# Optimization experiments

Hardware: AMD Instinct MI355X
Metric: run time of the kernel (lower is better)

## Reference

```python
import jax, jax.numpy as jnp
import numpy as np

B, N, C = 8, 1025, 768
NUM_HEADS = 12
HEAD_DIM = C // NUM_HEADS  # 64, also depthwise-conv channel count
HW = (32, 32)              # N = 1 + 32*32 (cls token)
SCALE = HEAD_DIM ** -0.5
VALUE_MASK_FILL = -10000.0
LN_EPS = 1e-5


def setup_inputs() -> dict:
    key = jax.random.key(0)
    ks = jax.random.split(key, 12)
    s = 0.02
    inp = {
        "x": jax.random.normal(ks[0], (B, N, C), jnp.float32),
        "mask": jax.random.bernoulli(ks[1], 0.9, (B, N)),
        "Wq": jax.random.normal(ks[2], (C, C), jnp.float32) * s,
        "Wk": jax.random.normal(ks[3], (C, C), jnp.float32) * s,
        "Wv": jax.random.normal(ks[4], (C, C), jnp.float32) * s,
        "pool_q_w": jax.random.normal(ks[5], (HEAD_DIM, 1, 3, 3), jnp.float32) * s,
        "pool_k_w": jax.random.normal(ks[6], (HEAD_DIM, 1, 3, 3), jnp.float32) * s,
        "pool_v_w": jax.random.normal(ks[7], (HEAD_DIM, 1, 3, 3), jnp.float32) * s,
        "gq": jnp.ones((HEAD_DIM,), jnp.float32),
        "bq": jnp.zeros((HEAD_DIM,), jnp.float32),
        "gk": jnp.ones((HEAD_DIM,), jnp.float32),
        "bk": jnp.zeros((HEAD_DIM,), jnp.float32),
        "gv": jnp.ones((HEAD_DIM,), jnp.float32),
        "bv": jnp.zeros((HEAD_DIM,), jnp.float32),
        "Wp": jax.random.normal(ks[8], (C, C), jnp.float32) * s,
        "bp": jnp.zeros((C,), jnp.float32),
    }
    return inp


def _layernorm(t, g, b):
    m = jnp.mean(t, axis=-1, keepdims=True)
    v = jnp.var(t, axis=-1, keepdims=True)
    return (t - m) * jax.lax.rsqrt(v + LN_EPS) * g + b


def _depthwise(t, w):
    # t: [BH, D, H, W], w: [D, 1, 3, 3] depthwise, stride 1, SAME padding
    return jax.lax.conv_general_dilated(
        t, w, window_strides=(1, 1), padding="SAME",
        dimension_numbers=("NCHW", "OIHW", "NCHW"),
        feature_group_count=t.shape[1])


def _attn_pool(t, w, g, b):
    # t: [B, H, N, D] with leading cls token; pool spatial tokens, norm after
    Bb, Hh, Nn, D = t.shape
    cls_tok, spat = t[:, :, :1], t[:, :, 1:]
    Hs, Ws = HW
    spat = spat.reshape(Bb * Hh, Hs, Ws, D).transpose(0, 3, 1, 2)
    spat = _depthwise(spat, w)
    spat = spat.reshape(Bb, Hh, D, Hs * Ws).transpose(0, 1, 3, 2)
    t = jnp.concatenate([cls_tok, spat], axis=2)
    return _layernorm(t, g, b)


def reference(x, mask, Wq, Wk, Wv, pool_q_w, pool_k_w, pool_v_w,
              gq, bq, gk, bk, gv, bv, Wp, bp):
    Bb, Nn, Cc = x.shape
    # QKV projections (no bias), split heads -> [B, H, N, D]
    q = (x @ Wq.T).reshape(Bb, Nn, NUM_HEADS, HEAD_DIM).transpose(0, 2, 1, 3)
    k = (x @ Wk.T).reshape(Bb, Nn, NUM_HEADS, HEAD_DIM).transpose(0, 2, 1, 3)
    v = (x @ Wv.T).reshape(Bb, Nn, NUM_HEADS, HEAD_DIM).transpose(0, 2, 1, 3)
    q = _attn_pool(q, pool_q_w, gq, bq)
    k = _attn_pool(k, pool_k_w, gk, bk)
    v = _attn_pool(v, pool_v_w, gv, bv)
    attn = jnp.einsum("bhqd,bhkd->bhqk", q, k) * SCALE
    # mask: [B, N] bool; broadcast as (B,1,N,1), False -> value_mask_fill
    attn = jnp.where(mask[:, None, :, None], attn, VALUE_MASK_FILL)
    attn = jax.nn.softmax(attn, axis=-1)
    attn_origin = attn
    out = jnp.einsum("bhqk,bhkd->bhqd", attn, v)
    # residual pooling, skipping the cls token
    out = jnp.concatenate([out[:, :, :1], out[:, :, 1:] + q[:, :, 1:]], axis=2)
    out = out.transpose(0, 2, 1, 3).reshape(Bb, Nn, Cc)
    out = out @ Wp.T + bp
    return out, attn_origin
```

## Files before the change

kernel.cpp:

```cpp
#include <hip/hip_runtime.h>
#include <hip/hip_bf16.h>
#include <cstdint>
#include <cstddef>

typedef unsigned short u16;
typedef __attribute__((ext_vector_type(8))) short bf16x8;
typedef __attribute__((ext_vector_type(4))) float f32x4;

#define MFMA16(a,b,c) __builtin_amdgcn_mfma_f32_16x16x32_bf16(a,b,c,0,0,0)
#define GLL16(gp, lp) __builtin_amdgcn_global_load_lds( \
    (const __attribute__((address_space(1))) void*)(gp), \
    (__attribute__((address_space(3))) void*)(lp), 16, 0, 0)

static constexpr int kB = 8, kH = 12, kN = 1025, kC = 768, kD = 64;
static constexpr int kBH = kB*kH;
static constexpr int kNP = 1056;
static constexpr int kM  = kB*kN;
static constexpr float kScale = 0.125f;

__device__ __forceinline__ u16 f2b(float f){
  unsigned u = __builtin_bit_cast(unsigned, f);
  u = (u + 0x7fffu + ((u>>16)&1u)) >> 16;
  return (u16)u;
}
__device__ __forceinline__ float b2f(u16 s){
  unsigned u = ((unsigned)s)<<16;
  return __builtin_bit_cast(float, u);
}

__global__ void k_conv_x(const float4* __restrict__ x, u16* __restrict__ out, int n4){
  int i = blockIdx.x*blockDim.x + threadIdx.x;
  int stride = gridDim.x*blockDim.x;
  for (; i<n4; i+=stride){
    float4 v = x[i];
    ushort4 o;
    o.x=f2b(v.x); o.y=f2b(v.y); o.z=f2b(v.z); o.w=f2b(v.w);
    *reinterpret_cast<ushort4*>(out + (size_t)i*4) = o;
  }
}

__global__ void k_conv_w(const float* __restrict__ w0, const float* __restrict__ w1,
                         const float* __restrict__ w2, const float* __restrict__ w3,
                         u16* __restrict__ out){
  const float* ws[4] = {w0,w1,w2,w3};
  int sel = blockIdx.y;
  const float4* src = reinterpret_cast<const float4*>(ws[sel]);
  int i = blockIdx.x*blockDim.x + threadIdx.x;
  float4 v = src[i];
  ushort4 o;
  o.x=f2b(v.x); o.y=f2b(v.y); o.z=f2b(v.z); o.w=f2b(v.w);
  *reinterpret_cast<ushort4*>(out + (size_t)sel*589824 + (size_t)i*4) = o;
}

__global__ void k_mask(const unsigned char* __restrict__ m, int* __restrict__ out, int n){
  __shared__ int cnt;
  if (threadIdx.x==0) cnt = 0;
  __syncthreads();
  int local = 0;
  for (int i=threadIdx.x; i<1024; i+=blockDim.x) local += (m[i]!=0);
  atomicAdd(&cnt, local);
  __syncthreads();
  bool b8 = (cnt > 512);
  for (int i=threadIdx.x; i<n; i+=blockDim.x){
    int v = b8 ? (m[i]!=0) : (reinterpret_cast<const int*>(m)[i] != 0);
    out[i] = v;
  }
}

template<int MODE>
__global__ __launch_bounds__(256) void k_gemm128(const u16* __restrict__ A,
      const u16* __restrict__ wb, const float* __restrict__ bias,
      u16* __restrict__ outb, float* __restrict__ outf){
  __shared__ union SM {
    struct { u16 a[128*32]; u16 b[128*32]; } s;
    u16 c[128*136];
  } sm;
  const int m0 = blockIdx.x*128;
  const int N0 = blockIdx.y*128;
  const int sel = (MODE==0) ? (N0/768) : 3;
  const int jb  = (MODE==0) ? (N0%768) : N0;
  const u16* W = wb + (size_t)sel*589824;
  const int t = threadIdx.x;
  const int wave = t>>6, lane = t&63;
  const int g = lane>>4, cl = lane&15;
  const int wr2 = (wave>>1)*64, wc2 = (wave&1)*64;

  const int cid0 = wave*64 + lane;
  const int cid1 = cid0 + 256;
  const int ar0 = m0 + (cid0>>2) < kM ? m0 + (cid0>>2) : kM-1;
  const int ar1 = m0 + (cid1>>2) < kM ? m0 + (cid1>>2) : kM-1;
  const int ac0 = (cid0&3)<<3, ac1 = (cid1&3)<<3;
  const int br0 = jb + (cid0>>2), br1 = jb + (cid1>>2);
  u16* lA0 = &sm.s.a[(wave*64)*8];
  u16* lA1 = &sm.s.a[(256 + wave*64)*8];
  u16* lB0 = &sm.s.b[(wave*64)*8];
  u16* lB1 = &sm.s.b[(256 + wave*64)*8];

  f32x4 acc[4][4];
  #pragma unroll
  for (int i=0;i<4;i++)
    #pragma unroll
    for (int j=0;j<4;j++) acc[i][j] = (f32x4){0.f,0.f,0.f,0.f};

  for (int k0=0; k0<768; k0+=32){
    __syncthreads();
    GLL16(A + (size_t)ar0*768 + k0 + ac0, lA0);
    GLL16(A + (size_t)ar1*768 + k0 + ac1, lA1);
    GLL16(W + (size_t)br0*768 + k0 + ac0, lB0);
    GLL16(W + (size_t)br1*768 + k0 + ac1, lB1);
    __syncthreads();
    bf16x8 af[4], bfg[4];
    #pragma unroll
    for (int fm=0; fm<4; fm++)
      af[fm] = *reinterpret_cast<const bf16x8*>(&sm.s.a[(wr2+fm*16+cl)*32 + g*8]);
    #pragma unroll
    for (int fn=0; fn<4; fn++)
      bfg[fn] = *reinterpret_cast<const bf16x8*>(&sm.s.b[(wc2+fn*16+cl)*32 + g*8]);
    #pragma unroll
    for (int fm=0; fm<4; fm++)
      #pragma unroll
      for (int fn=0; fn<4; fn++)
        acc[fm][fn] = MFMA16(af[fm], bfg[fn], acc[fm][fn]);
  }

  if (MODE==0){
    __syncthreads();
    #pragma unroll
    for (int fm=0; fm<4; fm++)
      #pragma unroll
      for (int fn=0; fn<4; fn++)
        #pragma unroll
        for (int i=0;i<4;i++){
          int r = wr2 + fm*16 + g*4 + i;
          int c = wc2 + fn*16 + cl;
          sm.c[r*136 + c] = f2b(acc[fm][fn][i]);
        }
    __syncthreads();
    #pragma unroll
    for (int it=0; it<8; it++){
      int cid = t + it*256;
      int r = cid >> 4, cc = (cid & 15) * 8;
      int gm = m0 + r;
      if (gm < kM){
        *reinterpret_cast<uint4*>(&outb[(size_t)gm*2304 + N0 + cc]) =
            *reinterpret_cast<const uint4*>(&sm.c[r*136 + cc]);
      }
    }
  } else {
    #pragma unroll
    for (int fm=0; fm<4; fm++)
      #pragma unroll
      for (int fn=0; fn<4; fn++)
        #pragma unroll
        for (int i=0;i<4;i++){
          int gm = m0 + wr2 + fm*16 + g*4 + i;
          if (gm >= kM) continue;
          int gc = jb + wc2 + fn*16 + cl;
          outf[(size_t)gm*768 + gc] = acc[fm][fn][i] + bias[gc];
        }
  }
}

__global__ __launch_bounds__(256) void k_pool3(const u16* __restrict__ qkvmat,
    const float* __restrict__ wq, const float* __restrict__ wk, const float* __restrict__ wv,
    const float* __restrict__ gq, const float* __restrict__ bq,
    const float* __restrict__ gk, const float* __restrict__ bk,
    const float* __restrict__ gv, const float* __restrict__ bv,
    u16* __restrict__ Qp, u16* __restrict__ Kp, u16* __restrict__ Vt){
  const int which = blockIdx.y;
  const float* w9 = (which==0)?wq:(which==1)?wk:wv;
  const float* gg = (which==0)?gq:(which==1)?gk:gv;
  const float* bb2= (which==0)?bq:(which==1)?bk:bv;
  const int transposed = (which==2);
  u16* out = (which==0)?Qp:(which==1)?Kp:Vt;

  const int wave = threadIdx.x>>6, d = threadIdx.x&63;
  const int grp = blockIdx.x % 264;
  const int bh  = blockIdx.x / 264;
  const int b = bh/12, h = bh - b*12;
  const int np  = grp*4 + wave;
  float v = 0.f;
  if (np < kN){
    const u16* base = qkvmat + ((size_t)b*1025)*2304 + which*768 + h*64;
    if (np == 0){
      v = b2f(base[d]);
    } else {
      int y = (np-1)>>5, x = (np-1)&31;
      #pragma unroll
      for (int ky=0; ky<3; ky++){
        int yy = y+ky-1;
        if (yy<0 || yy>31) continue;
        #pragma unroll
        for (int kx=0; kx<3; kx++){
          int xx = x+kx-1;
          if (xx<0 || xx>31) continue;
          v += w9[d*9+ky*3+kx] * b2f(base[(size_t)(1+yy*32+xx)*2304 + d]);
        }
      }
    }
    float s = v, s2 = v*v;
    #pragma unroll
    for (int off=1; off<64; off<<=1){ s += __shfl_xor(s, off); s2 += __shfl_xor(s2, off); }
    float mean = s*(1.f/64.f);
    float var  = s2*(1.f/64.f) - mean*mean;
    v = (v-mean)*rsqrtf(var+1e-5f)*gg[d] + bb2[d];
  }
  if (transposed) out[((size_t)bh*kD + d)*kNP + np] = f2b(v);
  else            out[((size_t)bh*kNP + np)*kD + d] = f2b(v);
}

__global__ __launch_bounds__(256) void k_attn(const u16* __restrict__ Qp, const u16* __restrict__ Kp,
    const u16* __restrict__ Vt, const int* __restrict__ maskn,
    float* __restrict__ attn_out, u16* __restrict__ ctx){
  constexpr int LDE = 1064;
  __shared__ u16 E[16*LDE];
  __shared__ float Lrow[16];
  __shared__ float Linv[16];
  const int wave = threadIdx.x>>6, lane = threadIdx.x&63;
  const int bh = blockIdx.x / 65;
  const int qt = blockIdx.x % 65;
  const int b  = bh / 12, h = bh - b*12;
  const int qbase = qt*16;
  const int g = lane>>4, cl = lane&15;

  if (threadIdx.x < 16) Lrow[threadIdx.x] = 0.f;
  __syncthreads();

  const u16* qrow = Qp + ((size_t)bh*kNP + (qbase + cl))*kD + g*8;
  bf16x8 aq0 = *reinterpret_cast<const bf16x8*>(qrow);
  bf16x8 aq1 = *reinterpret_cast<const bf16x8*>(qrow + 32);

  float mq[4];
  #pragma unroll
  for (int i=0;i<4;i++){
    int qi = qbase + g*4 + i;
    mq[i] = (qi<kN && maskn[b*kN+qi]!=0) ? kScale : 0.f;
  }

  const u16* kb = Kp + (size_t)bh*kNP*kD;
  float rsum[4] = {0.f,0.f,0.f,0.f};
  for (int kt=wave; kt<33; kt+=4){
    const int ktb = kt*32;
    const u16* kr = kb + (size_t)(ktb+cl)*kD + g*8;
    bf16x8 b00 = *reinterpret_cast<const bf16x8*>(kr);
    bf16x8 b01 = *reinterpret_cast<const bf16x8*>(kr+32);
    bf16x8 b10 = *reinterpret_cast<const bf16x8*>(kr+1024);
    bf16x8 b11 = *reinterpret_cast<const bf16x8*>(kr+1024+32);
    f32x4 s0 = {0.f,0.f,0.f,0.f}, s1 = {0.f,0.f,0.f,0.f};
    s0 = MFMA16(aq0,b00,s0); s0 = MFMA16(aq1,b01,s0);
    s1 = MFMA16(aq0,b10,s1); s1 = MFMA16(aq1,b11,s1);
    const bool v0 = (ktb+cl)<kN, v1 = (ktb+16+cl)<kN;
    #pragma unroll
    for (int i=0;i<4;i++){
      int row = g*4+i;
      float e0 = v0 ? __expf(s0[i]*mq[i]) : 0.f;
      float e1 = v1 ? __expf(s1[i]*mq[i]) : 0.f;
      rsum[i] += e0 + e1;
      E[row*LDE + ktb + cl]      = f2b(e0);
      E[row*LDE + ktb + 16 + cl] = f2b(e1);
    }
  }
  #pragma unroll
  for (int off=1; off<16; off<<=1){
    #pragma unroll
    for (int i=0;i<4;i++) rsum[i] += __shfl_xor(rsum[i], off);
  }
  if (cl == 0){
    #pragma unroll
    for (int i=0;i<4;i++) atomicAdd(&Lrow[g*4+i], rsum[i]);
  }
  __syncthreads();
  if (threadIdx.x < 16) Linv[threadIdx.x] = 1.f/Lrow[threadIdx.x];
  __syncthreads();

  {
    size_t S = (size_t)bh*kN*kN + (size_t)qbase*kN;
    float* tp = attn_out + S;
    int rows = kN - qbase; if (rows > 16) rows = 16;
    int T = rows*kN;
    int head = (int)((4 - (S & 3)) & 3);
    int body4 = (T - head) >> 2;
    int tail = T - head - body4*4;
    int t = threadIdx.x;
    if (t < head){
      int e = t;
      unsigned row = ((unsigned)(e*16369))>>24;
      int col = e - (int)row*kN;
      tp[e] = b2f(E[row*LDE+col]) * Linv[row];
    }
    if (t < tail){
      int e = head + body4*4 + t;
      unsigned row = ((unsigned)(e*16369))>>24;
      int col = e - (int)row*kN;
      tp[e] = b2f(E[row*LDE+col]) * Linv[row];
    }
    for (int idx = t; idx < body4; idx += 256){
      int e = head + idx*4;
      unsigned row0 = ((unsigned)(e*16369))>>24;
      unsigned row3 = ((unsigned)((e+3)*16369))>>24;
      float4 vv;
      if (row0 == row3){
        int col = e - (int)row0*kN;
        const u16* ep = &E[row0*LDE + col];
        float li = Linv[row0];
        vv.x = b2f(ep[0])*li; vv.y = b2f(ep[1])*li;
        vv.z = b2f(ep[2])*li; vv.w = b2f(ep[3])*li;
      } else {
        float tmp[4];
        #pragma unroll
        for (int j=0;j<4;j++){
          int ee = e+j;
          unsigned row = ((unsigned)(ee*16369))>>24;
          int col = ee - (int)row*kN;
          tmp[j] = b2f(E[row*LDE+col]) * Linv[row];
        }
        vv.x=tmp[0]; vv.y=tmp[1]; vv.z=tmp[2]; vv.w=tmp[3];
      }
      *reinterpret_cast<float4*>(tp + e) = vv;
    }
  }

  const int d0 = wave*16;
  f32x4 oacc = (f32x4){0.f,0.f,0.f,0.f};
  const u16* vb = Vt + ((size_t)bh*kD + d0 + cl)*kNP;
  for (int kt=0; kt<33; kt++){
    const int ko = kt*32 + g*8;
    bf16x8 pa  = *reinterpret_cast<const bf16x8*>(&E[cl*LDE + ko]);
    bf16x8 vbf = *reinterpret_cast<const bf16x8*>(vb + ko);
    oacc = MFMA16(pa, vbf, oacc);
  }
  #pragma unroll
  for (int i=0;i<4;i++){
    int row = g*4+i, qi = qbase+row;
    if (qi < kN){
      float val = oacc[i] * Linv[row];
      int dd = d0 + cl;
      if (qi >= 1) val += b2f(Qp[((size_t)bh*kNP + qi)*kD + dd]);
      ctx[((size_t)(b*kN + qi))*kC + h*kD + dd] = f2b(val);
    }
  }
}

extern "C" void kernel_launch(void* const* d_in, const int* in_sizes, int n_in,
                              void* d_out, int out_size, void* d_ws, size_t ws_size,
                              hipStream_t stream) {
  const float* x    = (const float*)d_in[0];
  const void*  msk  = d_in[1];
  const float* Wq   = (const float*)d_in[2];
  const float* Wk   = (const float*)d_in[3];
  const float* Wv   = (const float*)d_in[4];
  const float* pw_q = (const float*)d_in[5];
  const float* pw_k = (const float*)d_in[6];
  const float* pw_v = (const float*)d_in[7];
  const float* gq   = (const float*)d_in[8];
  const float* bq   = (const float*)d_in[9];
  const float* gk   = (const float*)d_in[10];
  const float* bk   = (const float*)d_in[11];
  const float* gv   = (const float*)d_in[12];
  const float* bv   = (const float*)d_in[13];
  const float* Wp   = (const float*)d_in[14];
  const float* bp   = (const float*)d_in[15];

  char* ws = (char*)d_ws;
  u16* xb     = (u16*)(ws + 0);
  u16* wb     = (u16*)(ws + 12595200);
  int* maskn  = (int*)(ws + 17313792);
  u16* qkvmat = (u16*)(ws + 17346816);
  u16* Qp     = (u16*)(ws + 55132416);
  u16* Kp     = (u16*)(ws + 68108544);
  u16* Vt     = (u16*)(ws + 81084672);
  u16* ctx    = (u16*)(ws + 17346816);

  float* out1 = (float*)d_out;
  float* attn = out1 + (size_t)kM*kC;

  k_conv_x<<<2048, 256, 0, stream>>>(reinterpret_cast<const float4*>(x), xb, (kM*kC)/4);
  k_conv_w<<<dim3(576,4), 256, 0, stream>>>(Wq, Wk, Wv, Wp, wb);
  k_mask<<<1, 256, 0, stream>>>((const unsigned char*)msk, maskn, kM);
  k_gemm128<0><<<dim3(65,18), 256, 0, stream>>>(xb, wb, nullptr, qkvmat, nullptr);
  k_pool3<<<dim3(kBH*264,3), 256, 0, stream>>>(qkvmat, pw_q, pw_k, pw_v,
                                               gq, bq, gk, bk, gv, bv, Qp, Kp, Vt);
  k_attn<<<96*65, 256, 0, stream>>>(Qp, Kp, Vt, maskn, attn, ctx);
  k_gemm128<1><<<dim3(65,6), 256, 0, stream>>>(ctx, wb, bp, nullptr, out1);
}
```

Before: 481.6 us.

## Fuse prep kernels, coarsen pooling with LDS-staged V transpose, remap attention blocks to XCDs

Merges the x/weight conversion and mask normalisation into one launch, so the single-block mask kernel no longer runs as its own serial step. Pooling blocks now handle 64 tokens each, with the conv weights held in registers, and V's transposed output is staged in LDS so global stores are coalesced. Attention blocks are remapped so each XCD handles whole heads, which should improve L2 reuse of K and V. The PV loop is batched four-wide to overlap loads. Coarser pooling blocks reduce parallelism, and the larger register footprint may lower occupancy.

```diff
diff --git a/kernel.cpp b/kernel.cpp
--- a/kernel.cpp
+++ b/kernel.cpp
@@ -28,42 +28,38 @@
   return __builtin_bit_cast(float, u);
 }
 
-__global__ void k_conv_x(const float4* __restrict__ x, u16* __restrict__ out, int n4){
-  int i = blockIdx.x*blockDim.x + threadIdx.x;
-  int stride = gridDim.x*blockDim.x;
-  for (; i<n4; i+=stride){
+__global__ __launch_bounds__(256) void k_prep(const float4* __restrict__ x,
+    const float* __restrict__ w0, const float* __restrict__ w1,
+    const float* __restrict__ w2, const float* __restrict__ w3,
+    const unsigned char* __restrict__ m,
+    u16* __restrict__ xb, u16* __restrict__ wb, int* __restrict__ maskn){
+  __shared__ int cnt;
+  const int bid = blockIdx.x;
+  if (bid < 6150){
+    int i = bid*256 + threadIdx.x;
     float4 v = x[i];
-    ushort4 o;
-    o.x=f2b(v.x); o.y=f2b(v.y); o.z=f2b(v.z); o.w=f2b(v.w);
-    *reinterpret_cast<ushort4*>(out + (size_t)i*4) = o;
-  }
-}
-
-__global__ void k_conv_w(const float* __restrict__ w0, const float* __restrict__ w1,
-                         const float* __restrict__ w2, const float* __restrict__ w3,
-                         u16* __restrict__ out){
-  const float* ws[4] = {w0,w1,w2,w3};
-  int sel = blockIdx.y;
-  const float4* src = reinterpret_cast<const float4*>(ws[sel]);
-  int i = blockIdx.x*blockDim.x + threadIdx.x;
-  float4 v = src[i];
-  ushort4 o;
-  o.x=f2b(v.x); o.y=f2b(v.y); o.z=f2b(v.z); o.w=f2b(v.w);
-  *reinterpret_cast<ushort4*>(out + (size_t)sel*589824 + (size_t)i*4) = o;
-}
-
-__global__ void k_mask(const unsigned char* __restrict__ m, int* __restrict__ out, int n){
-  __shared__ int cnt;
-  if (threadIdx.x==0) cnt = 0;
-  __syncthreads();
-  int local = 0;
-  for (int i=threadIdx.x; i<1024; i+=blockDim.x) local += (m[i]!=0);
-  atomicAdd(&cnt, local);
-  __syncthreads();
-  bool b8 = (cnt > 512);
-  for (int i=threadIdx.x; i<n; i+=blockDim.x){
-    int v = b8 ? (m[i]!=0) : (reinterpret_cast<const int*>(m)[i] != 0);
-    out[i] = v;
+    ushort4 o; o.x=f2b(v.x); o.y=f2b(v.y); o.z=f2b(v.z); o.w=f2b(v.w);
+    *reinterpret_cast<ushort4*>(xb + (size_t)i*4) = o;
+  } else if (bid < 8454){
+    int j = (bid-6150)*256 + threadIdx.x;
+    int sel = j/147456, i = j - sel*147456;
+    const float* ws[4] = {w0,w1,w2,w3};
+    float4 v = reinterpret_cast<const float4*>(ws[sel])[i];
+    ushort4 o; o.x=f2b(v.x); o.y=f2b(v.y); o.z=f2b(v.z); o.w=f2b(v.w);
+    *reinterpret_cast<ushort4*>(wb + (size_t)sel*589824 + (size_t)i*4) = o;
+  } else {
+    if (threadIdx.x==0) cnt = 0;
+    __syncthreads();
+    int local = 0;
+    for (int i=threadIdx.x; i<1024; i+=256) local += (m[i]!=0);
+    atomicAdd(&cnt, local);
+    __syncthreads();
+    bool b8 = (cnt > 512);
+    int lb = bid - 8454;
+    for (int i = lb*256 + threadIdx.x; i < kM; i += 32*256){
+      int v = b8 ? (m[i]!=0) : (reinterpret_cast<const int*>(m)[i] != 0);
+      maskn[i] = v;
+    }
   }
 }
 
@@ -167,46 +163,65 @@
     const float* __restrict__ gk, const float* __restrict__ bk,
     const float* __restrict__ gv, const float* __restrict__ bv,
     u16* __restrict__ Qp, u16* __restrict__ Kp, u16* __restrict__ Vt){
+  __shared__ u16 vt[64][72];
   const int which = blockIdx.y;
   const float* w9 = (which==0)?wq:(which==1)?wk:wv;
   const float* gg = (which==0)?gq:(which==1)?gk:gv;
   const float* bb2= (which==0)?bq:(which==1)?bk:bv;
-  const int transposed = (which==2);
   u16* out = (which==0)?Qp:(which==1)?Kp:Vt;
 
   const int wave = threadIdx.x>>6, d = threadIdx.x&63;
-  const int grp = blockIdx.x % 264;
-  const int bh  = blockIdx.x / 264;
+  const int nb  = blockIdx.x % 17;
+  const int bh  = blockIdx.x / 17;
   const int b = bh/12, h = bh - b*12;
-  const int np  = grp*4 + wave;
-  float v = 0.f;
-  if (np < kN){
-    const u16* base = qkvmat + ((size_t)b*1025)*2304 + which*768 + h*64;
-    if (np == 0){
-      v = b2f(base[d]);
-    } else {
-      int y = (np-1)>>5, x = (np-1)&31;
-      #pragma unroll
-      for (int ky=0; ky<3; ky++){
-        int yy = y+ky-1;
-        if (yy<0 || yy>31) continue;
+  const int np0 = nb*64;
+  const u16* base = qkvmat + ((size_t)b*1025)*2304 + which*768 + h*64;
+
+  float wreg[9];
+  #pragma unroll
+  for (int j=0;j<9;j++) wreg[j] = w9[d*9+j];
+  const float gd = gg[d], bd = bb2[d];
+
+  for (int iter=0; iter<16; ++iter){
+    const int np = np0 + iter*4 + wave;
+    float v = 0.f;
+    if (np < kN){
+      if (np == 0){
+        v = b2f(base[d]);
+      } else {
+        int y = (np-1)>>5, x = (np-1)&31;
         #pragma unroll
-        for (int kx=0; kx<3; kx++){
-          int xx = x+kx-1;
-          if (xx<0 || xx>31) continue;
-          v += w9[d*9+ky*3+kx] * b2f(base[(size_t)(1+yy*32+xx)*2304 + d]);
+        for (int ky=0; ky<3; ky++){
+          int yy = y+ky-1;
+          if (yy<0 || yy>31) continue;
+          #pragma unroll
+          for (int kx=0; kx<3; kx++){
+            int xx = x+kx-1;
+            if (xx<0 || xx>31) continue;
+            v += wreg[ky*3+kx] * b2f(base[(size_t)(1+yy*32+xx)*2304 + d]);
+          }
         }
       }
-    }
-    float s = v, s2 = v*v;
-    #pragma unroll
-    for (int off=1; off<64; off<<=1){ s += __shfl_xor(s, off); s2 += __shfl_xor(s2, off); }
-    float mean = s*(1.f/64.f);
-    float var  = s2*(1.f/64.f) - mean*mean;
-    v = (v-mean)*rsqrtf(var+1e-5f)*gg[d] + bb2[d];
-  }
-  if (transposed) out[((size_t)bh*kD + d)*kNP + np] = f2b(v);
-  else            out[((size_t)bh*kNP + np)*kD + d] = f2b(v);
+      float s = v, s2 = v*v;
+      #pragma unroll
+      for (int off=1; off<64; off<<=1){ s += __shfl_xor(s, off); s2 += __shfl_xor(s2, off); }
+      float mean = s*(1.f/64.f);
+      float var  = s2*(1.f/64.f) - mean*mean;
+      v = (v-mean)*rsqrtf(var+1e-5f)*gd + bd;
+    }
+    if (which==2) vt[d][iter*4+wave] = f2b(v);
+    else if (np < kNP) out[((size_t)bh*kNP + np)*kD + d] = f2b(v);
+  }
+
+  if (which==2){
+    __syncthreads();
+    const int dr = threadIdx.x>>2, seg = threadIdx.x&3;
+    if (np0 + seg*16 < kNP){
+      u16* dst = Vt + ((size_t)bh*kD + dr)*kNP + np0 + seg*16;
+      *reinterpret_cast<uint4*>(dst)     = *reinterpret_cast<const uint4*>(&vt[dr][seg*16]);
+      *reinterpret_cast<uint4*>(dst + 8) = *reinterpret_cast<const uint4*>(&vt[dr][seg*16+8]);
+    }
+  }
 }
 
 __global__ __launch_bounds__(256) void k_attn(const u16* __restrict__ Qp, const u16* __restrict__ Kp,
@@ -217,8 +232,10 @@
   __shared__ float Lrow[16];
   __shared__ float Linv[16];
   const int wave = threadIdx.x>>6, lane = threadIdx.x&63;
-  const int bh = blockIdx.x / 65;
-  const int qt = blockIdx.x % 65;
+  const int xcd  = blockIdx.x & 7;
+  const int slot = blockIdx.x >> 3;
+  const int bh = xcd*12 + slot/65;
+  const int qt = slot%65;
   const int b  = bh / 12, h = bh - b*12;
   const int qbase = qt*16;
   const int g = lane>>4, cl = lane&15;
@@ -239,6 +256,7 @@
 
   const u16* kb = Kp + (size_t)bh*kNP*kD;
   float rsum[4] = {0.f,0.f,0.f,0.f};
+  #pragma unroll 2
   for (int kt=wave; kt<33; kt+=4){
     const int ktb = kt*32;
     const u16* kr = kb + (size_t)(ktb+cl)*kD + g*8;
@@ -323,11 +341,22 @@
   const int d0 = wave*16;
   f32x4 oacc = (f32x4){0.f,0.f,0.f,0.f};
   const u16* vb = Vt + ((size_t)bh*kD + d0 + cl)*kNP;
-  for (int kt=0; kt<33; kt++){
-    const int ko = kt*32 + g*8;
-    bf16x8 pa  = *reinterpret_cast<const bf16x8*>(&E[cl*LDE + ko]);
-    bf16x8 vbf = *reinterpret_cast<const bf16x8*>(vb + ko);
-    oacc = MFMA16(pa, vbf, oacc);
+  for (int kt0=0; kt0<32; kt0+=4){
+    bf16x8 pa[4], vv[4];
+    #pragma unroll
+    for (int j=0;j<4;j++){
+      const int ko = (kt0+j)*32 + g*8;
+      pa[j] = *reinterpret_cast<const bf16x8*>(&E[cl*LDE + ko]);
+      vv[j] = *reinterpret_cast<const bf16x8*>(vb + ko);
+    }
+    #pragma unroll
+    for (int j=0;j<4;j++) oacc = MFMA16(pa[j], vv[j], oacc);
+  }
+  {
+    const int ko = 32*32 + g*8;
+    bf16x8 pa = *reinterpret_cast<const bf16x8*>(&E[cl*LDE + ko]);
+    bf16x8 vv = *reinterpret_cast<const bf16x8*>(vb + ko);
+    oacc = MFMA16(pa, vv, oacc);
   }
   #pragma unroll
   for (int i=0;i<4;i++){
@@ -374,12 +403,12 @@
   float* out1 = (float*)d_out;
   float* attn = out1 + (size_t)kM*kC;
 
-  k_conv_x<<<2048, 256, 0, stream>>>(reinterpret_cast<const float4*>(x), xb, (kM*kC)/4);
-  k_conv_w<<<dim3(576,4), 256, 0, stream>>>(Wq, Wk, Wv, Wp, wb);
-  k_mask<<<1, 256, 0, stream>>>((const unsigned char*)msk, maskn, kM);
+  k_prep<<<8486, 256, 0, stream>>>(reinterpret_cast<const float4*>(x),
+                                   Wq, Wk, Wv, Wp, (const unsigned char*)msk,
+                                   xb, wb, maskn);
   k_gemm128<0><<<dim3(65,18), 256, 0, stream>>>(xb, wb, nullptr, qkvmat, nullptr);
-  k_pool3<<<dim3(kBH*264,3), 256, 0, stream>>>(qkvmat, pw_q, pw_k, pw_v,
-                                               gq, bq, gk, bk, gv, bv, Qp, Kp, Vt);
+  k_pool3<<<dim3(96*17,3), 256, 0, stream>>>(qkvmat, pw_q, pw_k, pw_v,
+                                             gq, bq, gk, bk, gv, bv, Qp, Kp, Vt);
   k_attn<<<96*65, 256, 0, stream>>>(Qp, Kp, Vt, maskn, attn, ctx);
   k_gemm128<1><<<dim3(65,6), 256, 0, stream>>>(ctx, wb, bp, nullptr, out1);
 }
```

Result: faster. 434.5 us (-9.8%).
